# Kernel tuning notes

Hardware: AMD Instinct MI355X
Metric: run time of the kernel (lower is better)

Reference implementation:

```python
import jax, jax.numpy as jnp
import numpy as np

B, S, H = 32, 255, 1024
BS, WD, O = 120, 20, 10
HSZ = 2 * (BS + 1) + WD  # 262


def setup_inputs() -> dict:
    key = jax.random.key(0)
    ks = jax.random.split(key, 9)
    inv = lambda *d: 1.0 / np.sqrt(d[0])
    return {
        "state": jax.random.normal(ks[0], (B, S, H), jnp.float32),
        "head_w": jax.random.normal(ks[1], (H, BS), jnp.float32) * inv(H),
        "head_b": jax.random.normal(ks[2], (BS,), jnp.float32) * 0.02,
        "tail_w": jax.random.normal(ks[3], (H, BS), jnp.float32) * inv(H),
        "tail_b": jax.random.normal(ks[4], (BS,), jnp.float32) * 0.02,
        "U": jax.random.normal(ks[5], (O, BS, BS), jnp.float32) * inv(BS),
        "width_table": jax.random.normal(ks[6], (256, WD), jnp.float32).at[0].set(0.0),  # padding_idx=0
        "cls_w": jax.random.normal(ks[7], (O, HSZ), jnp.float32) * inv(HSZ),
        "cls_b": jax.random.normal(ks[8], (O,), jnp.float32) * 0.02,
    }


def _leaky_relu(x):
    return jnp.where(x >= 0, x, 0.01 * x)  # torch LeakyReLU default slope


def reference(state, head_w, head_b, tail_w, tail_b, U, width_table, cls_w, cls_b):
    b, s, _ = state.shape
    bs = head_w.shape[1]
    # head/tail MLPs (dropout is identity in eval)
    h = _leaky_relu(state @ head_w + head_b)  # (b, s, bs)
    t = _leaky_relu(state @ tail_w + tail_b)  # (b, s, bs)

    # bilinear term
    scores1 = jnp.einsum('bxi,oij,byj->bxyo', h, U, t)  # (b, s, s, O)

    # append bias-ones feature
    ones = jnp.ones((b, s, 1), h.dtype)
    h1 = jnp.concatenate([h, ones], axis=-1)  # (b, s, bs+1)
    t1 = jnp.concatenate([t, ones], axis=-1)

    # span-width embedding: pos[x, y] = y - x + 1, clamped to 0 for y < x
    pos = jnp.arange(s)[None, :] - jnp.arange(s)[:, None] + 1
    pos = pos * (pos > 0)
    wemb = width_table[pos]  # (s, s, WD)

    # cls(concat(h1_x, t1_y, wemb_xy)) decomposed into three small projections
    # + broadcast-add; mathematically identical to materializing affined_cat.
    Wh = cls_w[:, :bs + 1]              # (O, bs+1)
    Wt = cls_w[:, bs + 1:2 * (bs + 1)]  # (O, bs+1)
    Ww = cls_w[:, 2 * (bs + 1):]        # (O, WD)
    scores2 = (jnp.einsum('bxi,oi->bxo', h1, Wh)[:, :, None, :]
               + jnp.einsum('byi,oi->byo', t1, Wt)[:, None, :, :]
               + jnp.einsum('xyw,ow->xyo', wemb, Ww)[None]
               + cls_b)
    return scores1 + scores2
```

## Files before the change

kernel.cpp:

```cpp
#include <hip/hip_runtime.h>
#include <hip/hip_bf16.h>

using f32x4 = __attribute__((ext_vector_type(4))) float;
using s16x8 = __attribute__((ext_vector_type(8))) short;
using s16x4 = __attribute__((ext_vector_type(4))) short;

constexpr int RTOT = 32 * 255;

__device__ inline unsigned short f2bf(float x) {
    __hip_bfloat16 b = __float2bfloat16(x);
    return __builtin_bit_cast(unsigned short, b);
}
__device__ inline float bf2f(unsigned short u) {
    unsigned int t = ((unsigned int)u) << 16;
    return __builtin_bit_cast(float, t);
}
__device__ inline f32x4 mfma16(s16x8 a, s16x8 b, f32x4 c) {
    return __builtin_amdgcn_mfma_f32_16x16x32_bf16(a, b, c, 0, 0, 0);
}
__device__ inline void gload16(const unsigned short* g, unsigned short* l) {
    __builtin_amdgcn_global_load_lds(
        (const __attribute__((address_space(1))) void*)g,
        (__attribute__((address_space(3))) void*)l, 16, 0, 0);
}


__global__ __launch_bounds__(256) void convert_k(
    const float* __restrict__ head_w, const float* __restrict__ tail_w,
    const float* __restrict__ U, const float* __restrict__ wtab,
    const float* __restrict__ cls_w,
    unsigned short* __restrict__ WP, unsigned short* __restrict__ Ut,
    float* __restrict__ tblp)
{
    const int tid = threadIdx.x;
    if (blockIdx.x < 16) {
        __shared__ unsigned short Lw[64][258];
        const int ks = blockIdx.x;
        for (int idx = tid; idx < 64 * 16; idx += 256) {
            int r = idx >> 4, c = idx & 15;
            Lw[r][120 + ((c >= 8) ? 128 : 0) + (c & 7)] = 0;
        }
        for (int idx = tid; idx < 7680; idx += 256) {
            int r = idx / 120, c = idx - r * 120;
            Lw[r][c] = f2bf(head_w[(ks * 64 + r) * 120 + c]);
        }
        for (int idx = tid; idx < 7680; idx += 256) {
            int r = idx / 120, c = idx - r * 120;
            Lw[r][128 + c] = f2bf(tail_w[(ks * 64 + r) * 120 + c]);
        }
        __syncthreads();
        for (int item = tid; item < 2048; item += 256) {
            int n = item >> 3, kcp = item & 7;
            int kc = kcp ^ (n & 7);
            s16x8 v;
            #pragma unroll
            for (int e = 0; e < 8; ++e) v[e] = (short)Lw[kc * 8 + e][n];
            *(s16x8*)&WP[ks * 16384 + item * 8] = v;
        }
    } else {
        int gid = (blockIdx.x - 16) * 256 + tid;
        if (gid < 163840) {
            int j = gid & 127, i2 = (gid >> 7) & 127, o = gid >> 14;
            float v = (i2 < 120 && j < 120) ? U[((size_t)o * 120 + i2) * 120 + j] : 0.f;
            Ut[(size_t)o * 16384 + (size_t)j * 128 + i2] = f2bf(v);
        } else {
            int id = gid - 163840;
            if (id < 2560) {
                int p = id / 10, o = id - (id / 10) * 10;
                float s = 0.f;
                #pragma unroll
                for (int wq = 0; wq < 20; ++wq)
                    s += wtab[p * 20 + wq] * cls_w[o * 262 + 242 + wq];
                tblp[p * 12 + o] = s;
            }
        }
    }
}

__global__ __launch_bounds__(512) void ht_mfma(
    const float* __restrict__ state, const unsigned short* __restrict__ WP,
    const unsigned short* __restrict__ Ut,
    const float* __restrict__ head_b, const float* __restrict__ tail_b,
    const float* __restrict__ cls_w, const float* __restrict__ cls_b,
    unsigned short* __restrict__ tbuf, unsigned short* __restrict__ hUb,
    float* __restrict__ hwp, float* __restrict__ twp)
{
    __shared__ unsigned short Ss[2][32 * 64];
    __shared__ unsigned short Ws[2][256 * 64];
    const int r0 = blockIdx.x * 32;
    const int tid = threadIdx.x;
    const int w = tid >> 6, lane = tid & 63;
    const int l16 = lane & 15, kq = lane >> 4;
    const int srow = (tid >> 3) & 31, skc = tid & 7;
    const bool do_s = tid < 256;
    const float* sp = &state[(size_t)(r0 + srow) * 1024 + skc * 8];

    f32x4 acc[2][2];
    #pragma unroll
    for (int fn = 0; fn < 2; ++fn)
        #pragma unroll
        for (int fr = 0; fr < 2; ++fr) acc[fn][fr] = (f32x4){0.f, 0.f, 0.f, 0.f};

    #pragma unroll
    for (int j = 0; j < 4; ++j) {
        int off = (w * 4 + j) * 512;
        gload16(WP + off + lane * 8, &Ws[0][off]);
    }
    if (do_s) {
        f32x4 a0 = *(const f32x4*)sp;
        f32x4 a1 = *(const f32x4*)(sp + 4);
        s16x8 pk;
        #pragma unroll
        for (int e = 0; e < 4; ++e) { pk[e] = (short)f2bf(a0[e]); pk[e + 4] = (short)f2bf(a1[e]); }
        *(s16x8*)((char*)&Ss[0][0] + srow * 128 + ((skc * 16) ^ ((srow & 7) << 4))) = pk;
    }
    __syncthreads();

    for (int it = 0; it < 16; ++it) {
        const int cur = it & 1;
        f32x4 a0, a1;
        if (it < 15) {
            #pragma unroll
            for (int j = 0; j < 4; ++j) {
                int off = (w * 4 + j) * 512;
                gload16(WP + (it + 1) * 16384 + off + lane * 8, &Ws[cur ^ 1][off]);
            }
            if (do_s) {
                a0 = *(const f32x4*)(sp + (it + 1) * 64);
                a1 = *(const f32x4*)(sp + (it + 1) * 64 + 4);
            }
        }
        const char* SsB = (const char*)&Ss[cur][0];
        const char* WsB = (const char*)&Ws[cur][0];
        s16x8 bf[2][2];
        #pragma unroll
        for (int fr = 0; fr < 2; ++fr) {
            int rr = fr * 16 + l16;
            #pragma unroll
            for (int ks = 0; ks < 2; ++ks)
                bf[fr][ks] = *(const s16x8*)(SsB + rr * 128 + ((ks * 64 + kq * 16) ^ ((rr & 7) << 4)));
        }
        #pragma unroll
        for (int fn = 0; fn < 2; ++fn) {
            int n = w * 32 + fn * 16 + l16;
            #pragma unroll
            for (int ks = 0; ks < 2; ++ks) {
                s16x8 af = *(const s16x8*)(WsB + n * 128 + ((ks * 64 + kq * 16) ^ ((n & 7) << 4)));
                #pragma unroll
                for (int fr = 0; fr < 2; ++fr)
                    acc[fn][fr] = mfma16(af, bf[fr][ks], acc[fn][fr]);
            }
        }
        if (it < 15 && do_s) {
            s16x8 pk;
            #pragma unroll
            for (int e = 0; e < 4; ++e) { pk[e] = (short)f2bf(a0[e]); pk[e + 4] = (short)f2bf(a1[e]); }
            *(s16x8*)((char*)&Ss[cur ^ 1][0] + srow * 128 + ((skc * 16) ^ ((srow & 7) << 4))) = pk;
        }
        __syncthreads();
    }

    unsigned short* Hl = &Ws[0][0];
    unsigned short* Tl = &Ws[1][0];
    #pragma unroll
    for (int fn = 0; fn < 2; ++fn) {
        const int n0 = w * 32 + fn * 16 + kq * 4;
        const int isT = n0 >= 128;
        const int c0 = n0 & 127;
        const int g = c0 >> 3, sub = c0 & 7;
        const float* bp = isT ? tail_b : head_b;
        unsigned short* dstl = isT ? Tl : Hl;
        #pragma unroll
        for (int fr = 0; fr < 2; ++fr) {
            const int rloc = fr * 16 + l16;
            const int r = r0 + rloc;
            s16x4 pk;
            #pragma unroll
            for (int e = 0; e < 4; ++e) {
                float bv = (c0 + e < 120) ? bp[c0 + e] : 0.f;
                float z = acc[fn][fr][e] + bv;
                z = (z >= 0.f) ? z : 0.01f * z;
                pk[e] = (short)f2bf(z);
            }
            *(s16x4*)&dstl[rloc * 128 + ((g ^ (rloc & 7)) << 3) + sub] = pk;
            if (isT) {
                int bq = r / 255, x = r - bq * 255;
                *(s16x4*)&tbuf[((size_t)bq * 256 + x) * 128 + ((g ^ (x & 7)) << 3) + sub] = pk;
            }
        }
    }
    __syncthreads();

    float* Wl = (float*)&Ws[0][4096];
    for (int idx = tid; idx < 2430; idx += 512) {
        if (idx < 2420) {
            int which = idx / 1210, rem = idx - which * 1210;
            int o = rem / 121, i = rem - o * 121;
            Wl[idx] = cls_w[o * 262 + which * 121 + i];
        } else Wl[idx] = cls_b[idx - 2420];
    }
    __syncthreads();

    {
        s16x8 bh[2][4];
        #pragma unroll
        for (int rf = 0; rf < 2; ++rf) {
            int rr = rf * 16 + l16;
            #pragma unroll
            for (int ks = 0; ks < 4; ++ks)
                bh[rf][ks] = *(const s16x8*)((const char*)Hl + rr * 256 +
                              ((ks * 64 + kq * 16) ^ ((rr & 7) << 4)));
        }
        size_t rbase[2]; int x4[2];
        #pragma unroll
        for (int rf = 0; rf < 2; ++rf) {
            int gr = r0 + rf * 16 + l16;
            int bq = gr / 255, x = gr - bq * 255;
            rbase[rf] = ((size_t)bq * 3072 + x * 12) * 128;
            x4[rf] = x * 4;
        }
        const int j = w * 16 + l16;
        const int j0 = w * 16 + kq * 4;
        const int g2 = j0 >> 3, sub2 = j0 & 7;
        for (int o = 0; o < 10; ++o) {
            f32x4 acc1[2];
            #pragma unroll
            for (int rf = 0; rf < 2; ++rf) acc1[rf] = (f32x4){0.f, 0.f, 0.f, 0.f};
            #pragma unroll
            for (int ks = 0; ks < 4; ++ks) {
                s16x8 af = *(const s16x8*)&Ut[(size_t)o * 16384 +
                            (size_t)j * 128 + ks * 32 + kq * 8];
                #pragma unroll
                for (int rf = 0; rf < 2; ++rf)
                    acc1[rf] = mfma16(af, bh[rf][ks], acc1[rf]);
            }
            #pragma unroll
            for (int rf = 0; rf < 2; ++rf) {
                int key = (x4[rf] + o) & 7;
                s16x4 pk;
                #pragma unroll
                for (int e = 0; e < 4; ++e) pk[e] = (short)f2bf(acc1[rf][e]);
                *(s16x4*)&hUb[rbase[rf] + (size_t)o * 128 + ((g2 ^ key) << 3) + sub2] = pk;
            }
        }
    }

    for (int d = tid; d < 640; d += 512) {
        int which = d / 320, rem = d - which * 320;
        int rr = rem / 10, o = rem - rr * 10;
        const unsigned short* row = (which ? Tl : Hl) + rr * 128;
        const float* wp2 = &Wl[which * 1210 + o * 121];
        float s = 0.f;
        #pragma unroll
        for (int c = 0; c < 15; ++c) {
            s16x8 v = *(const s16x8*)&row[(c ^ (rr & 7)) << 3];
            #pragma unroll
            for (int e = 0; e < 8; ++e)
                s += bf2f((unsigned short)v[e]) * wp2[c * 8 + e];
        }
        s += wp2[120];
        int gr = r0 + rr;
        if (!which) hwp[(size_t)gr * 12 + o] = s + Wl[2420 + o];
        else        twp[(size_t)gr * 12 + o] = s;
    }
}

__global__ __launch_bounds__(512) void main_mfma(
    const unsigned short* __restrict__ hU, const unsigned short* __restrict__ tbuf,
    const float* __restrict__ hwp, const float* __restrict__ twp,
    const float* __restrict__ tblp, float* __restrict__ out)
{
    __shared__ unsigned short Bs[256 * 128];
    __shared__ unsigned short As[2][128 * 128];
    __shared__ float Ts[3060];
    __shared__ float Tb[3072];
    __shared__ float Hw[384];
    const int wgid = blockIdx.x + (blockIdx.y << 3);
    const int virt = (wgid & 7) * 32 + (wgid >> 3);
    const int b = virt >> 3, mg = virt & 7;
    const int tid = threadIdx.x;
    const int w = tid >> 6, lane = tid & 63;
    const int l16 = lane & 15, kq = lane >> 4;
    const int wm = w >> 2, wy = w & 3;
    const size_t hUbase = (size_t)b * 3072 * 128;
    const size_t tbase = (size_t)b * 256 * 128;

    #pragma unroll
    for (int j = 0; j < 8; ++j) {
        int off = (w * 8 + j) * 512;
        gload16(&tbuf[tbase + off + lane * 8], &Bs[off]);
    }
    {
        const size_t a0 = hUbase + (size_t)(mg * 3 * 128) * 128;
        #pragma unroll
        for (int j = 0; j < 4; ++j) {
            int off = (w * 4 + j) * 512;
            gload16(&hU[a0 + off + lane * 8], &As[0][off]);
        }
    }
    {
        const float* twb = twp + (size_t)b * 3060;
        for (int idx = tid; idx < 3060; idx += 512) Ts[idx] = twb[idx];
        for (int idx = tid; idx < 3072; idx += 512) Tb[idx] = tblp[idx];
        if (tid < 384 && mg * 384 + tid < 3060)
            Hw[tid] = hwp[(size_t)b * 3060 + mg * 384 + tid];
    }
    __syncthreads();

    s16x8 bfr[4][4];
    #pragma unroll
    for (int ks = 0; ks < 4; ++ks)
        #pragma unroll
        for (int fy = 0; fy < 4; ++fy) {
            int row = wy * 64 + fy * 16 + l16;
            bfr[ks][fy] = *(const s16x8*)((const char*)Bs + row * 256 +
                           ((ks * 64 + kq * 16) ^ ((row & 7) << 4)));
        }

    for (int i = 0; i < 3; ++i) {
        const int m0 = (mg * 3 + i) * 128;
        if (i < 2) {
            const size_t an = hUbase + (size_t)(m0 + 128) * 128;
            #pragma unroll
            for (int j = 0; j < 4; ++j) {
                int off = (w * 4 + j) * 512;
                gload16(&hU[an + off + lane * 8], &As[(i + 1) & 1][off]);
            }
        }
        const char* AsB = (const char*)&As[i & 1][0];
        f32x4 acc[4][4];
        #pragma unroll
        for (int fm = 0; fm < 4; ++fm)
            #pragma unroll
            for (int fy = 0; fy < 4; ++fy) acc[fm][fy] = (f32x4){0.f, 0.f, 0.f, 0.f};

        __builtin_amdgcn_s_setprio(1);
        #pragma unroll
        for (int ks = 0; ks < 4; ++ks) {
            s16x8 af[4];
            #pragma unroll
            for (int fm = 0; fm < 4; ++fm) {
                int row = wm * 64 + fm * 16 + l16;
                af[fm] = *(const s16x8*)(AsB + row * 256 +
                          ((ks * 64 + kq * 16) ^ ((row & 7) << 4)));
            }
            #pragma unroll
            for (int fm = 0; fm < 4; ++fm)
                #pragma unroll
                for (int fy = 0; fy < 4; ++fy)
                    acc[fm][fy] = mfma16(af[fm], bfr[ks][fy], acc[fm][fy]);
        }
        __builtin_amdgcn_s_setprio(0);

        __syncthreads();

        #pragma unroll
        for (int fm = 0; fm < 4; ++fm) {
            const int ml = m0 + wm * 64 + fm * 16 + kq * 4;
            if (ml < 3060) {
                const int x = ml / 12, o0 = ml % 12;
                const int rx = b * 255 + x;
                f32x4 hv = *(const f32x4*)&Hw[(x - mg * 32) * 12 + o0];
                #pragma unroll
                for (int fy = 0; fy < 4; ++fy) {
                    const int y = wy * 64 + fy * 16 + l16;
                    if (y < 255) {
                        f32x4 tv = *(const f32x4*)&Ts[y * 12 + o0];
                        int p = y - x + 1; if (p < 0) p = 0;
                        f32x4 wv = *(const f32x4*)&Tb[p * 12 + o0];
                        float* op = &out[((size_t)rx * 255 + y) * 10 + o0];
                        if (o0 < 8) {
                            float v[4];
                            #pragma unroll
                            for (int e = 0; e < 4; ++e)
                                v[e] = acc[fm][fy][e] + hv[e] + tv[e] + wv[e];
                            __builtin_memcpy(op, v, 16);
                        } else {
                            float v[2];
                            v[0] = acc[fm][fy][0] + hv[0] + tv[0] + wv[0];
                            v[1] = acc[fm][fy][1] + hv[1] + tv[1] + wv[1];
                            __builtin_memcpy(op, v, 8);
                        }
                    }
                }
            }
        }
    }
}

extern "C" void kernel_launch(void* const* d_in, const int* in_sizes, int n_in,
                              void* d_out, int out_size, void* d_ws, size_t ws_size,
                              hipStream_t stream)
{
    (void)in_sizes; (void)n_in; (void)out_size; (void)ws_size;
    const float* state  = (const float*)d_in[0];
    const float* head_w = (const float*)d_in[1];
    const float* head_b = (const float*)d_in[2];
    const float* tail_w = (const float*)d_in[3];
    const float* tail_b = (const float*)d_in[4];
    const float* U      = (const float*)d_in[5];
    const float* wtab   = (const float*)d_in[6];
    const float* cls_w  = (const float*)d_in[7];
    const float* cls_b  = (const float*)d_in[8];
    float* out = (float*)d_out;

    unsigned short* u16 = (unsigned short*)d_ws;
    unsigned short* tbuf = u16;
    unsigned short* hUb  = tbuf + 1048576;
    unsigned short* WP   = hUb + 12582912;
    unsigned short* Ut   = WP + 262144;
    float* hwp  = (float*)(Ut + 163840);
    float* twp  = hwp + 97920;
    float* tblp = twp + 97920;

    hipLaunchKernelGGL(convert_k, dim3(666), dim3(256), 0, stream,
                       head_w, tail_w, U, wtab, cls_w, WP, Ut, tblp);
    hipLaunchKernelGGL(ht_mfma, dim3(255), dim3(512), 0, stream,
                       state, WP, Ut, head_b, tail_b, cls_w, cls_b,
                       tbuf, hUb, hwp, twp);
    hipLaunchKernelGGL(main_mfma, dim3(8, 32), dim3(512), 0, stream,
                       hUb, tbuf, hwp, twp, tblp, out);
}
```

Baseline: 79.85 us.

## Fuse h·U projection into main kernel, computing hU in shared memory

The h·U bilinear projection moves out of ht_mfma, which now writes a plain bf16 head buffer. main_mfma computes hU for its 32 rows directly into LDS, where the main MFMA loop then reads it. This removes the large hU write and read-back through global memory, along with the per-iteration async double-buffered loads. In exchange, main_mfma uses more LDS (about 124 KB) and does extra MFMA work before its main loop, which may lower occupancy and serialize that phase.

```diff
diff --git a/kernel.cpp b/kernel.cpp
--- a/kernel.cpp
+++ b/kernel.cpp
@@ -79,10 +79,9 @@
 
 __global__ __launch_bounds__(512) void ht_mfma(
     const float* __restrict__ state, const unsigned short* __restrict__ WP,
-    const unsigned short* __restrict__ Ut,
     const float* __restrict__ head_b, const float* __restrict__ tail_b,
     const float* __restrict__ cls_w, const float* __restrict__ cls_b,
-    unsigned short* __restrict__ tbuf, unsigned short* __restrict__ hUb,
+    unsigned short* __restrict__ hbuf, unsigned short* __restrict__ tbuf,
     float* __restrict__ hwp, float* __restrict__ twp)
 {
     __shared__ unsigned short Ss[2][32 * 64];
@@ -170,6 +169,7 @@
         const int g = c0 >> 3, sub = c0 & 7;
         const float* bp = isT ? tail_b : head_b;
         unsigned short* dstl = isT ? Tl : Hl;
+        unsigned short* dstg = isT ? tbuf : hbuf;
         #pragma unroll
         for (int fr = 0; fr < 2; ++fr) {
             const int rloc = fr * 16 + l16;
@@ -183,9 +183,9 @@
                 pk[e] = (short)f2bf(z);
             }
             *(s16x4*)&dstl[rloc * 128 + ((g ^ (rloc & 7)) << 3) + sub] = pk;
-            if (isT) {
+            {
                 int bq = r / 255, x = r - bq * 255;
-                *(s16x4*)&tbuf[((size_t)bq * 256 + x) * 128 + ((g ^ (x & 7)) << 3) + sub] = pk;
+                *(s16x4*)&dstg[((size_t)bq * 256 + x) * 128 + ((g ^ (x & 7)) << 3) + sub] = pk;
             }
         }
     }
@@ -201,50 +201,6 @@
     }
     __syncthreads();
 
-    {
-        s16x8 bh[2][4];
-        #pragma unroll
-        for (int rf = 0; rf < 2; ++rf) {
-            int rr = rf * 16 + l16;
-            #pragma unroll
-            for (int ks = 0; ks < 4; ++ks)
-                bh[rf][ks] = *(const s16x8*)((const char*)Hl + rr * 256 +
-                              ((ks * 64 + kq * 16) ^ ((rr & 7) << 4)));
-        }
-        size_t rbase[2]; int x4[2];
-        #pragma unroll
-        for (int rf = 0; rf < 2; ++rf) {
-            int gr = r0 + rf * 16 + l16;
-            int bq = gr / 255, x = gr - bq * 255;
-            rbase[rf] = ((size_t)bq * 3072 + x * 12) * 128;
-            x4[rf] = x * 4;
-        }
-        const int j = w * 16 + l16;
-        const int j0 = w * 16 + kq * 4;
-        const int g2 = j0 >> 3, sub2 = j0 & 7;
-        for (int o = 0; o < 10; ++o) {
-            f32x4 acc1[2];
-            #pragma unroll
-            for (int rf = 0; rf < 2; ++rf) acc1[rf] = (f32x4){0.f, 0.f, 0.f, 0.f};
-            #pragma unroll
-            for (int ks = 0; ks < 4; ++ks) {
-                s16x8 af = *(const s16x8*)&Ut[(size_t)o * 16384 +
-                            (size_t)j * 128 + ks * 32 + kq * 8];
-                #pragma unroll
-                for (int rf = 0; rf < 2; ++rf)
-                    acc1[rf] = mfma16(af, bh[rf][ks], acc1[rf]);
-            }
-            #pragma unroll
-            for (int rf = 0; rf < 2; ++rf) {
-                int key = (x4[rf] + o) & 7;
-                s16x4 pk;
-                #pragma unroll
-                for (int e = 0; e < 4; ++e) pk[e] = (short)f2bf(acc1[rf][e]);
-                *(s16x4*)&hUb[rbase[rf] + (size_t)o * 128 + ((g2 ^ key) << 3) + sub2] = pk;
-            }
-        }
-    }
-
     for (int d = tid; d < 640; d += 512) {
         int which = d / 320, rem = d - which * 320;
         int rr = rem / 10, o = rem - rr * 10;
@@ -266,15 +222,19 @@
 }
 
 __global__ __launch_bounds__(512) void main_mfma(
-    const unsigned short* __restrict__ hU, const unsigned short* __restrict__ tbuf,
+    const unsigned short* __restrict__ hbuf, const unsigned short* __restrict__ tbuf,
+    const unsigned short* __restrict__ Ut,
     const float* __restrict__ hwp, const float* __restrict__ twp,
     const float* __restrict__ tblp, float* __restrict__ out)
 {
-    __shared__ unsigned short Bs[256 * 128];
-    __shared__ unsigned short As[2][128 * 128];
-    __shared__ float Ts[3060];
-    __shared__ float Tb[3072];
-    __shared__ float Hw[384];
+    __shared__ __align__(16) char smem[124416];
+    unsigned short* hUs = (unsigned short*)smem;
+    unsigned short* Bs  = (unsigned short*)smem;
+    unsigned short* Hs  = (unsigned short*)(smem + 65536);
+    float* Ts = (float*)(smem + 98304);
+    float* Tb = (float*)(smem + 110592);
+    float* Hw = (float*)(smem + 122880);
+
     const int wgid = blockIdx.x + (blockIdx.y << 3);
     const int virt = (wgid & 7) * 32 + (wgid >> 3);
     const int b = virt >> 3, mg = virt & 7;
@@ -282,28 +242,23 @@
     const int w = tid >> 6, lane = tid & 63;
     const int l16 = lane & 15, kq = lane >> 4;
     const int wm = w >> 2, wy = w & 3;
-    const size_t hUbase = (size_t)b * 3072 * 128;
     const size_t tbase = (size_t)b * 256 * 128;
+    const size_t hbase = ((size_t)b * 256 + mg * 32) * 128;
 
     #pragma unroll
     for (int j = 0; j < 8; ++j) {
         int off = (w * 8 + j) * 512;
         gload16(&tbuf[tbase + off + lane * 8], &Bs[off]);
     }
-    {
-        const size_t a0 = hUbase + (size_t)(mg * 3 * 128) * 128;
-        #pragma unroll
-        for (int j = 0; j < 4; ++j) {
-            int off = (w * 4 + j) * 512;
-            gload16(&hU[a0 + off + lane * 8], &As[0][off]);
-        }
-    }
+    gload16(&hbuf[hbase + (size_t)(w * 64 + lane) * 8], &Hs[w * 512]);
     {
         const float* twb = twp + (size_t)b * 3060;
         for (int idx = tid; idx < 3060; idx += 512) Ts[idx] = twb[idx];
         for (int idx = tid; idx < 3072; idx += 512) Tb[idx] = tblp[idx];
-        if (tid < 384 && mg * 384 + tid < 3060)
-            Hw[tid] = hwp[(size_t)b * 3060 + mg * 384 + tid];
+        if (tid < 384) {
+            int mgl = mg * 384 + tid;
+            Hw[tid] = (mgl < 3060) ? hwp[(size_t)b * 3060 + mgl] : 0.f;
+        }
     }
     __syncthreads();
 
@@ -316,18 +271,48 @@
             bfr[ks][fy] = *(const s16x8*)((const char*)Bs + row * 256 +
                            ((ks * 64 + kq * 16) ^ ((row & 7) << 4)));
         }
+    s16x8 bh[2][4];
+    #pragma unroll
+    for (int xf = 0; xf < 2; ++xf) {
+        int rr = xf * 16 + l16;
+        #pragma unroll
+        for (int ks = 0; ks < 4; ++ks)
+            bh[xf][ks] = *(const s16x8*)((const char*)Hs + rr * 256 +
+                          ((ks * 64 + kq * 16) ^ ((rr & 7) << 4)));
+    }
+    __syncthreads();
+
+    {
+        const int jrow = w * 16 + l16;
+        const int j0 = w * 16 + kq * 4;
+        const int g2 = j0 >> 3, sub2b = (j0 & 7) * 2;
+        #pragma unroll 2
+        for (int o = 0; o < 10; ++o) {
+            f32x4 acc1[2];
+            acc1[0] = (f32x4){0.f, 0.f, 0.f, 0.f};
+            acc1[1] = (f32x4){0.f, 0.f, 0.f, 0.f};
+            #pragma unroll
+            for (int ks = 0; ks < 4; ++ks) {
+                s16x8 af = *(const s16x8*)&Ut[(size_t)o * 16384 +
+                            (size_t)jrow * 128 + ks * 32 + kq * 8];
+                acc1[0] = mfma16(af, bh[0][ks], acc1[0]);
+                acc1[1] = mfma16(af, bh[1][ks], acc1[1]);
+            }
+            #pragma unroll
+            for (int xf = 0; xf < 2; ++xf) {
+                int mloc = (xf * 16 + l16) * 12 + o;
+                s16x4 pk;
+                #pragma unroll
+                for (int e = 0; e < 4; ++e) pk[e] = (short)f2bf(acc1[xf][e]);
+                *(s16x4*)((char*)hUs + mloc * 256 +
+                          ((g2 ^ (mloc & 7)) << 4) + sub2b) = pk;
+            }
+        }
+    }
+    __syncthreads();
 
     for (int i = 0; i < 3; ++i) {
-        const int m0 = (mg * 3 + i) * 128;
-        if (i < 2) {
-            const size_t an = hUbase + (size_t)(m0 + 128) * 128;
-            #pragma unroll
-            for (int j = 0; j < 4; ++j) {
-                int off = (w * 4 + j) * 512;
-                gload16(&hU[an + off + lane * 8], &As[(i + 1) & 1][off]);
-            }
-        }
-        const char* AsB = (const char*)&As[i & 1][0];
+        const int mt = i * 128;
         f32x4 acc[4][4];
         #pragma unroll
         for (int fm = 0; fm < 4; ++fm)
@@ -340,8 +325,8 @@
             s16x8 af[4];
             #pragma unroll
             for (int fm = 0; fm < 4; ++fm) {
-                int row = wm * 64 + fm * 16 + l16;
-                af[fm] = *(const s16x8*)(AsB + row * 256 +
+                int row = mt + wm * 64 + fm * 16 + l16;
+                af[fm] = *(const s16x8*)((const char*)hUs + row * 256 +
                           ((ks * 64 + kq * 16) ^ ((row & 7) << 4)));
             }
             #pragma unroll
@@ -352,15 +337,14 @@
         }
         __builtin_amdgcn_s_setprio(0);
 
-        __syncthreads();
-
         #pragma unroll
         for (int fm = 0; fm < 4; ++fm) {
-            const int ml = m0 + wm * 64 + fm * 16 + kq * 4;
-            if (ml < 3060) {
-                const int x = ml / 12, o0 = ml % 12;
+            const int mloc = mt + wm * 64 + fm * 16 + kq * 4;
+            const int xloc = mloc / 12, o0 = mloc % 12;
+            const int x = mg * 32 + xloc;
+            if (x < 255) {
                 const int rx = b * 255 + x;
-                f32x4 hv = *(const f32x4*)&Hw[(x - mg * 32) * 12 + o0];
+                f32x4 hv = *(const f32x4*)&Hw[xloc * 12 + o0];
                 #pragma unroll
                 for (int fy = 0; fy < 4; ++fy) {
                     const int y = wy * 64 + fy * 16 + l16;
@@ -406,8 +390,8 @@
 
     unsigned short* u16 = (unsigned short*)d_ws;
     unsigned short* tbuf = u16;
-    unsigned short* hUb  = tbuf + 1048576;
-    unsigned short* WP   = hUb + 12582912;
+    unsigned short* hbuf = tbuf + 1048576;
+    unsigned short* WP   = hbuf + 1048576;
     unsigned short* Ut   = WP + 262144;
     float* hwp  = (float*)(Ut + 163840);
     float* twp  = hwp + 97920;
@@ -416,8 +400,8 @@
     hipLaunchKernelGGL(convert_k, dim3(666), dim3(256), 0, stream,
                        head_w, tail_w, U, wtab, cls_w, WP, Ut, tblp);
     hipLaunchKernelGGL(ht_mfma, dim3(255), dim3(512), 0, stream,
-                       state, WP, Ut, head_b, tail_b, cls_w, cls_b,
-                       tbuf, hUb, hwp, twp);
+                       state, WP, head_b, tail_b, cls_w, cls_b,
+                       hbuf, tbuf, hwp, twp);
     hipLaunchKernelGGL(main_mfma, dim3(8, 32), dim3(512), 0, stream,
-                       hUb, tbuf, hwp, twp, tblp, out);
-}
+                       hbuf, tbuf, Ut, hwp, twp, tblp, out);
+}
```

Result: faster. 76.16 us (-4.6%).
